# Optimization experiments

Hardware: AMD Instinct MI355X
Metric: run time of the kernel (lower is better)

The kernel has to match this reference:

```python
import jax, jax.numpy as jnp
import numpy as np

TOP_K = 2


def setup_inputs() -> dict:
    key = jax.random.key(0)
    ks = jax.random.split(key, 5)
    B, S, D, F, E = 2, 1024, 2048, 4096, 8
    scale_in = 1.0 / np.sqrt(D)
    scale_f = 1.0 / np.sqrt(F)
    return {
        "hidden_states": jax.random.normal(ks[0], (B, S, D), dtype=jnp.float32),
        "gate_w": jax.random.normal(ks[1], (D, E), dtype=jnp.float32) * scale_in,
        "w1": jax.random.normal(ks[2], (E, D, F), dtype=jnp.float32) * scale_in,
        "w3": jax.random.normal(ks[3], (E, D, F), dtype=jnp.float32) * scale_in,
        "w2": jax.random.normal(ks[4], (E, F, D), dtype=jnp.float32) * scale_f,
    }


def reference(hidden_states, gate_w, w1, w3, w2):
    orig_shape = hidden_states.shape
    D = orig_shape[-1]
    x = hidden_states.reshape(-1, D)                      # [T, D]
    E = gate_w.shape[-1]

    # Router: replicated linear (no bias), logits in fp32.
    router_logits = (x @ gate_w).astype(jnp.float32)      # [T, E]
    probs = jax.nn.softmax(router_logits, axis=-1)        # [T, E]
    topk_vals, topk_idx = jax.lax.top_k(probs, TOP_K)     # [T, K]
    # renormalize=False: use raw softmax probs of the selected experts.
    # Scatter top-k weights back to a dense [T, E] combine matrix.
    onehot = jax.nn.one_hot(topk_idx, E, dtype=probs.dtype)        # [T, K, E]
    combine = jnp.einsum("tke,tk->te", onehot, topk_vals)          # [T, E]

    # Dense-over-experts SwiGLU (reference for the fused grouped-GEMM).
    gate = jax.nn.silu(jnp.einsum("td,edf->etf", x, w1))  # [E, T, F]
    up = jnp.einsum("td,edf->etf", x, w3)                 # [E, T, F]
    expert_out = jnp.einsum("etf,efd->etd", gate * up, w2)  # [E, T, D]

    # Combine (this is the TP all-reduce + weighted sum in vllm).
    y = jnp.einsum("te,etd->td", combine, expert_out)     # [T, D]
    return y.reshape(orig_shape)
```

## Files before the change

### kernel.cpp

```cpp
#include <hip/hip_runtime.h>

typedef short v8s __attribute__((ext_vector_type(8)));
typedef float v4f __attribute__((ext_vector_type(4)));
typedef float v16f __attribute__((ext_vector_type(16)));

#define T_TOK 2048
#define DD 2048
#define FF 4096
#define EE 8
#define BM 128
#define BN 128
#define BK 64
#define MT_MAX 40
#define MAXROWS 5120

#define WS_COUNTS 0
#define WS_FILL   32
#define WS_ROWOFF 64
#define WS_TOPE   128
#define WS_TOPW   (WS_TOPE + T_TOK * 2 * 4)
#define WS_IDS    (WS_TOPW + T_TOK * 2 * 4)
#define WS_WTS    (WS_IDS + MAXROWS * 4)
#define WS_ZERO   (WS_WTS + MAXROWS * 4)
#define WS_XB     73984ul
#define WS_H      (WS_XB + 8388608ul)

#define SW(r)     ((((r) ^ ((r) >> 3)) & 7))
#define SWZ(r, kb) ((r) * 128 + ((kb) ^ (SW(r) << 4)))

#define VMCNTN(N) asm volatile("s_waitcnt vmcnt(" #N ")" ::: "memory")
#define VMCNT0()  asm volatile("s_waitcnt vmcnt(0)" ::: "memory")
#define LGKM0()   asm volatile("s_waitcnt lgkmcnt(0)" ::: "memory")
#define BARR()    __builtin_amdgcn_s_barrier()
#define SCHEDB()  __builtin_amdgcn_sched_barrier(0)

static __device__ __forceinline__ short f2bf(float f) {
  return __builtin_bit_cast(short, static_cast<__bf16>(f));
}

static __device__ __forceinline__ void gload_lds16(const void* g, void* l) {
  __builtin_amdgcn_global_load_lds(
      (const __attribute__((address_space(1))) unsigned int*)g,
      (__attribute__((address_space(3))) unsigned int*)l, 16, 0, 0);
}

__global__ __launch_bounds__(256) void xbf_k(const float* __restrict__ x,
                                             unsigned short* __restrict__ xb) {
  const int i = (blockIdx.x * 256 + threadIdx.x) * 8;
  v4f a = *(const v4f*)(x + i);
  v4f b = *(const v4f*)(x + i + 4);
  v8s h;
  h[0] = f2bf(a[0]); h[1] = f2bf(a[1]); h[2] = f2bf(a[2]); h[3] = f2bf(a[3]);
  h[4] = f2bf(b[0]); h[5] = f2bf(b[1]); h[6] = f2bf(b[2]); h[7] = f2bf(b[3]);
  *(v8s*)(xb + i) = h;
}

__global__ __launch_bounds__(256) void router_k(
    const float* __restrict__ x, const float* __restrict__ gw,
    int* __restrict__ counts, int* __restrict__ tope, float* __restrict__ topw) {
  const int lane = threadIdx.x & 63;
  const int t = blockIdx.x * 4 + (threadIdx.x >> 6);
  if (t >= T_TOK) return;
  float acc[EE] = {0.f, 0.f, 0.f, 0.f, 0.f, 0.f, 0.f, 0.f};
  const float* xr = x + (size_t)t * DD;
  for (int i = 0; i < DD / 64; ++i) {
    int k = i * 64 + lane;
    float xv = xr[k];
    const v4f* g = (const v4f*)(gw + (size_t)k * EE);
    v4f g0 = g[0], g1 = g[1];
    acc[0] += xv * g0[0]; acc[1] += xv * g0[1]; acc[2] += xv * g0[2]; acc[3] += xv * g0[3];
    acc[4] += xv * g1[0]; acc[5] += xv * g1[1]; acc[6] += xv * g1[2]; acc[7] += xv * g1[3];
  }
  #pragma unroll
  for (int e = 0; e < EE; ++e) {
    #pragma unroll
    for (int off = 32; off > 0; off >>= 1) acc[e] += __shfl_xor(acc[e], off);
  }
  if (lane == 0) {
    float m = acc[0];
    #pragma unroll
    for (int e = 1; e < EE; ++e) m = fmaxf(m, acc[e]);
    float p[EE], s = 0.f;
    #pragma unroll
    for (int e = 0; e < EE; ++e) { p[e] = expf(acc[e] - m); s += p[e]; }
    float inv = 1.f / s;
    #pragma unroll
    for (int e = 0; e < EE; ++e) p[e] *= inv;
    int e1 = 0;
    #pragma unroll
    for (int e = 1; e < EE; ++e) if (p[e] > p[e1]) e1 = e;
    int e2 = (e1 == 0) ? 1 : 0;
    #pragma unroll
    for (int e = 0; e < EE; ++e) if (e != e1 && p[e] > p[e2]) e2 = e;
    tope[2 * t] = e1;  tope[2 * t + 1] = e2;
    topw[2 * t] = p[e1]; topw[2 * t + 1] = p[e2];
    atomicAdd(&counts[e1], 1);
    atomicAdd(&counts[e2], 1);
  }
}

__global__ void offsets_k(const int* __restrict__ counts, int* __restrict__ rowoff) {
  if (threadIdx.x == 0) {
    int off = 0;
    #pragma unroll
    for (int e = 0; e < EE; ++e) {
      rowoff[e] = off;
      off += ((counts[e] + BM - 1) / BM) * BM;
    }
  }
}

__global__ __launch_bounds__(256) void scatter_k(
    const int* __restrict__ tope, const float* __restrict__ topw,
    const int* __restrict__ rowoff, int* __restrict__ fill,
    int* __restrict__ ids, float* __restrict__ wts) {
  const int t = blockIdx.x * 256 + threadIdx.x;
  if (t >= T_TOK) return;
  #pragma unroll
  for (int j = 0; j < 2; ++j) {
    int e = tope[2 * t + j];
    int pos = rowoff[e] + atomicAdd(&fill[e], 1);
    ids[pos] = t;
    wts[pos] = topw[2 * t + j];
  }
}

static __device__ __forceinline__ int find_expert(
    const int* counts, const int* rowoff, int mt) {
  int expert = -1;
  #pragma unroll
  for (int e = 0; e < EE; ++e) {
    int rs = rowoff[e];
    int tl = (counts[e] + BM - 1) / BM;
    if (mt * BM >= rs && mt * BM < rs + tl * BM) expert = e;
  }
  return expert;
}

static __device__ __forceinline__ void xcd_map(int* nt, int* mt) {
  int gx = gridDim.x, gy = gridDim.y;
  int nwg = gx * gy;
  int lin = blockIdx.y * gx + blockIdx.x;
  int q = nwg >> 3;
  int s = (lin & 7) * q + (lin >> 3);
  *nt = s / gy;
  *mt = s % gy;
}

__global__ __launch_bounds__(256, 2) void gemm1_k(
    const unsigned short* __restrict__ xb, const float* __restrict__ w1,
    const float* __restrict__ w3, const int* __restrict__ counts,
    const int* __restrict__ rowoff, const int* __restrict__ ids,
    unsigned short* __restrict__ H) {
  int nt, mt;
  xcd_map(&nt, &mt);
  const int expert = find_expert(counts, rowoff, mt);
  if (expert < 0) return;
  const int m0 = mt * BM, n0 = nt * BN;

  __shared__ unsigned short sA[BM * BK];
  __shared__ unsigned short sB0[BN * BK];
  __shared__ unsigned short sB1[BN * BK];

  const int tid = threadIdx.x;
  const int lane = tid & 63;
  const int wid = tid >> 6;
  const int wm = (wid >> 1) * 64, wn = (wid & 1) * 64;
  const int l32 = lane & 31;
  const int khi = lane >> 5;

  const unsigned short* ga[4];
  #pragma unroll
  for (int i = 0; i < 4; ++i) {
    int r = wid * 32 + i * 8 + (lane >> 3);
    ga[i] = xb + (size_t)ids[m0 + r] * DD + (((lane & 7) ^ SW(r)) << 3);
  }

  const int b_f4 = (tid & 31) * 4;
  const int b_k8 = (tid >> 5) * 8;
  const float* wb1 = w1 + (size_t)expert * DD * FF + n0 + b_f4 + (size_t)b_k8 * FF;
  const float* wb3 = w3 + (size_t)expert * DD * FF + n0 + b_f4 + (size_t)b_k8 * FF;

  v4f r1[8], r3[8];
  #define G1_ALDS(KT) { _Pragma("unroll") for (int i_ = 0; i_ < 4; ++i_)        \
      gload_lds16(ga[i_] + (size_t)(KT) * BK,                                   \
                  (char*)sA + (wid * 32 + i_ * 8) * 128); }
  #define G1_BL(KT) {                                                           \
      const float* p_ = wb1 + (size_t)(KT) * BK * FF;                           \
      _Pragma("unroll") for (int j_ = 0; j_ < 8; ++j_)                          \
        r1[j_] = *(const v4f*)(p_ + (size_t)j_ * FF);                           \
      p_ = wb3 + (size_t)(KT) * BK * FF;                                        \
      _Pragma("unroll") for (int j_ = 0; j_ < 8; ++j_)                          \
        r3[j_] = *(const v4f*)(p_ + (size_t)j_ * FF); }
  #define G1_BW() { _Pragma("unroll") for (int c_ = 0; c_ < 4; ++c_) {          \
      v8s h1_, h3_;                                                             \
      _Pragma("unroll") for (int j_ = 0; j_ < 8; ++j_) {                        \
        h1_[j_] = f2bf(r1[j_][c_]); h3_[j_] = f2bf(r3[j_][c_]); }               \
      *(v8s*)((char*)sB0 + SWZ(b_f4 + c_, b_k8 * 2)) = h1_;                     \
      *(v8s*)((char*)sB1 + SWZ(b_f4 + c_, b_k8 * 2)) = h3_; } }

  v16f acc1[2][2], acc3[2][2];
  #pragma unroll
  for (int i = 0; i < 2; ++i)
    #pragma unroll
    for (int j = 0; j < 2; ++j) {
      acc1[i][j] = (v16f)(0.f);
      acc3[i][j] = (v16f)(0.f);
    }

  G1_BL(0);

  for (int kt = 0; kt < DD / BK; ++kt) {
    G1_ALDS(kt);
    SCHEDB();
    G1_BW();
    if (kt + 1 < DD / BK) {
      G1_BL(kt + 1);
      SCHEDB();
      VMCNTN(16);
    } else {
      VMCNT0();
    }
    LGKM0(); BARR();
    SCHEDB();
    #pragma unroll
    for (int ks = 0; ks < 4; ++ks) {
      const int kb = (ks * 2 + khi) * 16;
      v8s a[2], b1[2], b3[2];
      #pragma unroll
      for (int m = 0; m < 2; ++m)
        a[m] = *(const v8s*)((const char*)sA + SWZ(wm + m * 32 + l32, kb));
      #pragma unroll
      for (int n = 0; n < 2; ++n) {
        b1[n] = *(const v8s*)((const char*)sB0 + SWZ(wn + n * 32 + l32, kb));
        b3[n] = *(const v8s*)((const char*)sB1 + SWZ(wn + n * 32 + l32, kb));
      }
      #pragma unroll
      for (int m = 0; m < 2; ++m)
        #pragma unroll
        for (int n = 0; n < 2; ++n) {
          acc1[m][n] = __builtin_amdgcn_mfma_f32_32x32x16_bf16(a[m], b1[n], acc1[m][n], 0, 0, 0);
          acc3[m][n] = __builtin_amdgcn_mfma_f32_32x32x16_bf16(a[m], b3[n], acc3[m][n], 0, 0, 0);
        }
    }
    BARR();
  }
  #pragma unroll
  for (int m = 0; m < 2; ++m)
    #pragma unroll
    for (int n = 0; n < 2; ++n)
      #pragma unroll
      for (int r = 0; r < 16; ++r) {
        int row = wm + m * 32 + (r & 3) + 8 * (r >> 2) + 4 * khi;
        int col = wn + n * 32 + l32;
        float g = acc1[m][n][r];
        float u = acc3[m][n][r];
        float hv = (g / (1.f + expf(-g))) * u;
        H[(size_t)(m0 + row) * FF + (n0 + col)] = (unsigned short)f2bf(hv);
      }
}

__global__ __launch_bounds__(256, 2) void gemm2_k(
    const unsigned short* __restrict__ H, const float* __restrict__ w2,
    const int* __restrict__ counts, const int* __restrict__ rowoff,
    const int* __restrict__ ids, const float* __restrict__ wts,
    float* __restrict__ out) {
  int nt, mt;
  xcd_map(&nt, &mt);
  const int expert = find_expert(counts, rowoff, mt);
  if (expert < 0) return;
  const int m0 = mt * BM, n0 = nt * BN;

  __shared__ unsigned short sA[BM * BK];
  __shared__ unsigned short sB[BN * BK];

  const int tid = threadIdx.x;
  const int lane = tid & 63;
  const int wid = tid >> 6;
  const int wm = (wid >> 1) * 64, wn = (wid & 1) * 64;
  const int l32 = lane & 31;
  const int khi = lane >> 5;

  const unsigned short* ga[4];
  #pragma unroll
  for (int i = 0; i < 4; ++i) {
    int r = wid * 32 + i * 8 + (lane >> 3);
    ga[i] = H + (size_t)(m0 + r) * FF + (((lane & 7) ^ SW(r)) << 3);
  }

  const int b_f4 = (tid & 31) * 4;
  const int b_k8 = (tid >> 5) * 8;
  const float* wb = w2 + (size_t)expert * FF * DD + n0 + b_f4 + (size_t)b_k8 * DD;

  v4f rb[8];
  #define G2_ALDS(KT) { _Pragma("unroll") for (int i_ = 0; i_ < 4; ++i_)        \
      gload_lds16(ga[i_] + (size_t)(KT) * BK,                                   \
                  (char*)sA + (wid * 32 + i_ * 8) * 128); }
  #define G2_BL(KT) { const float* p_ = wb + (size_t)(KT) * BK * DD;            \
      _Pragma("unroll") for (int j_ = 0; j_ < 8; ++j_)                          \
        rb[j_] = *(const v4f*)(p_ + (size_t)j_ * DD); }
  #define G2_BW() { _Pragma("unroll") for (int c_ = 0; c_ < 4; ++c_) {          \
      v8s h_;                                                                   \
      _Pragma("unroll") for (int j_ = 0; j_ < 8; ++j_) h_[j_] = f2bf(rb[j_][c_]);\
      *(v8s*)((char*)sB + SWZ(b_f4 + c_, b_k8 * 2)) = h_; } }

  v16f acc[2][2];
  #pragma unroll
  for (int i = 0; i < 2; ++i)
    #pragma unroll
    for (int j = 0; j < 2; ++j) acc[i][j] = (v16f)(0.f);

  G2_BL(0);

  for (int kt = 0; kt < FF / BK; ++kt) {
    G2_ALDS(kt);
    SCHEDB();
    G2_BW();
    if (kt + 1 < FF / BK) {
      G2_BL(kt + 1);
      SCHEDB();
      VMCNTN(8);
    } else {
      VMCNT0();
    }
    LGKM0(); BARR();
    SCHEDB();
    #pragma unroll
    for (int ks = 0; ks < 4; ++ks) {
      const int kb = (ks * 2 + khi) * 16;
      v8s a[2], b[2];
      #pragma unroll
      for (int m = 0; m < 2; ++m)
        a[m] = *(const v8s*)((const char*)sA + SWZ(wm + m * 32 + l32, kb));
      #pragma unroll
      for (int n = 0; n < 2; ++n)
        b[n] = *(const v8s*)((const char*)sB + SWZ(wn + n * 32 + l32, kb));
      #pragma unroll
      for (int m = 0; m < 2; ++m)
        #pragma unroll
        for (int n = 0; n < 2; ++n)
          acc[m][n] = __builtin_amdgcn_mfma_f32_32x32x16_bf16(a[m], b[n], acc[m][n], 0, 0, 0);
    }
    BARR();
  }
  #pragma unroll
  for (int m = 0; m < 2; ++m)
    #pragma unroll
    for (int r = 0; r < 16; ++r) {
      int row = m0 + wm + m * 32 + (r & 3) + 8 * (r >> 2) + 4 * khi;
      float wgt = wts[row];
      if (wgt != 0.f) {
        float* orow = out + (size_t)ids[row] * DD + n0 + wn + l32;
        #pragma unroll
        for (int n = 0; n < 2; ++n)
          atomicAdd(orow + n * 32, wgt * acc[m][n][r]);
      }
    }
}

extern "C" void kernel_launch(void* const* d_in, const int* in_sizes, int n_in,
                              void* d_out, int out_size, void* d_ws, size_t ws_size,
                              hipStream_t stream) {
  const float* x  = (const float*)d_in[0];
  const float* gw = (const float*)d_in[1];
  const float* w1 = (const float*)d_in[2];
  const float* w3 = (const float*)d_in[3];
  const float* w2 = (const float*)d_in[4];
  float* out = (float*)d_out;
  char* ws = (char*)d_ws;

  int*   counts = (int*)(ws + WS_COUNTS);
  int*   fill   = (int*)(ws + WS_FILL);
  int*   rowoff = (int*)(ws + WS_ROWOFF);
  int*   tope   = (int*)(ws + WS_TOPE);
  float* topw   = (float*)(ws + WS_TOPW);
  int*   ids    = (int*)(ws + WS_IDS);
  float* wts    = (float*)(ws + WS_WTS);
  unsigned short* xb = (unsigned short*)(ws + WS_XB);
  unsigned short* H  = (unsigned short*)(ws + WS_H);

  hipMemsetAsync(ws, 0, WS_ZERO, stream);
  hipMemsetAsync(d_out, 0, (size_t)out_size * sizeof(float), stream);

  xbf_k<<<T_TOK * DD / (256 * 8), 256, 0, stream>>>(x, xb);
  router_k<<<T_TOK / 4, 256, 0, stream>>>(x, gw, counts, tope, topw);
  offsets_k<<<1, 64, 0, stream>>>(counts, rowoff);
  scatter_k<<<T_TOK / 256, 256, 0, stream>>>(tope, topw, rowoff, fill, ids, wts);
  gemm1_k<<<dim3(FF / BN, MT_MAX), 256, 0, stream>>>(xb, w1, w3, counts, rowoff, ids, H);
  gemm2_k<<<dim3(DD / BN, MT_MAX), 256, 0, stream>>>(H, w2, counts, rowoff, ids, wts, out);
}
```

Baseline: 514.2 us.

## Replace gemm2 atomic scatter with bf16 staging buffer and combine kernel

gemm2 now writes each expert-row's output as bf16 into a dense staging buffer O instead of doing weighted float atomicAdds into the output. A new combine kernel reads each token's two slots (recorded by scatter) and computes the weighted sum, which also removes the output memset. This trades atomic contention for an extra kernel launch plus roughly 20 MB of extra write and read traffic, and rounds expert outputs to bf16 before combining.

```diff
diff --git a/kernel.cpp b/kernel.cpp
--- a/kernel.cpp
+++ b/kernel.cpp
@@ -22,13 +22,16 @@
 #define WS_IDS    (WS_TOPW + T_TOK * 2 * 4)
 #define WS_WTS    (WS_IDS + MAXROWS * 4)
 #define WS_ZERO   (WS_WTS + MAXROWS * 4)
-#define WS_XB     73984ul
+#define WS_SLOT   73856ul
+#define WS_XB     90368ul
 #define WS_H      (WS_XB + 8388608ul)
-
-#define SW(r)     ((((r) ^ ((r) >> 3)) & 7))
+#define WS_O      (WS_H + 41943040ul)
+
+#define SW(r)      ((((r) ^ ((r) >> 3)) & 7))
 #define SWZ(r, kb) ((r) * 128 + ((kb) ^ (SW(r) << 4)))
 
-#define VMCNTN(N) asm volatile("s_waitcnt vmcnt(" #N ")" ::: "memory")
+#define VMCNT16() asm volatile("s_waitcnt vmcnt(16)" ::: "memory")
+#define VMCNT8()  asm volatile("s_waitcnt vmcnt(8)" ::: "memory")
 #define VMCNT0()  asm volatile("s_waitcnt vmcnt(0)" ::: "memory")
 #define LGKM0()   asm volatile("s_waitcnt lgkmcnt(0)" ::: "memory")
 #define BARR()    __builtin_amdgcn_s_barrier()
@@ -36,6 +39,9 @@
 
 static __device__ __forceinline__ short f2bf(float f) {
   return __builtin_bit_cast(short, static_cast<__bf16>(f));
+}
+static __device__ __forceinline__ float bf2f(unsigned short u) {
+  return __builtin_bit_cast(float, ((unsigned)u) << 16);
 }
 
 static __device__ __forceinline__ void gload_lds16(const void* g, void* l) {
@@ -113,7 +119,7 @@
 __global__ __launch_bounds__(256) void scatter_k(
     const int* __restrict__ tope, const float* __restrict__ topw,
     const int* __restrict__ rowoff, int* __restrict__ fill,
-    int* __restrict__ ids, float* __restrict__ wts) {
+    int* __restrict__ ids, float* __restrict__ wts, int* __restrict__ slot) {
   const int t = blockIdx.x * 256 + threadIdx.x;
   if (t >= T_TOK) return;
   #pragma unroll
@@ -122,6 +128,7 @@
     int pos = rowoff[e] + atomicAdd(&fill[e], 1);
     ids[pos] = t;
     wts[pos] = topw[2 * t + j];
+    slot[2 * t + j] = pos;
   }
 }
 
@@ -217,7 +224,7 @@
     if (kt + 1 < DD / BK) {
       G1_BL(kt + 1);
       SCHEDB();
-      VMCNTN(16);
+      VMCNT16();
     } else {
       VMCNT0();
     }
@@ -263,8 +270,7 @@
 __global__ __launch_bounds__(256, 2) void gemm2_k(
     const unsigned short* __restrict__ H, const float* __restrict__ w2,
     const int* __restrict__ counts, const int* __restrict__ rowoff,
-    const int* __restrict__ ids, const float* __restrict__ wts,
-    float* __restrict__ out) {
+    unsigned short* __restrict__ O) {
   int nt, mt;
   xcd_map(&nt, &mt);
   const int expert = find_expert(counts, rowoff, mt);
@@ -319,7 +325,7 @@
     if (kt + 1 < FF / BK) {
       G2_BL(kt + 1);
       SCHEDB();
-      VMCNTN(8);
+      VMCNT8();
     } else {
       VMCNT0();
     }
@@ -343,19 +349,37 @@
     }
     BARR();
   }
+
   #pragma unroll
   for (int m = 0; m < 2; ++m)
     #pragma unroll
     for (int r = 0; r < 16; ++r) {
       int row = m0 + wm + m * 32 + (r & 3) + 8 * (r >> 2) + 4 * khi;
-      float wgt = wts[row];
-      if (wgt != 0.f) {
-        float* orow = out + (size_t)ids[row] * DD + n0 + wn + l32;
-        #pragma unroll
-        for (int n = 0; n < 2; ++n)
-          atomicAdd(orow + n * 32, wgt * acc[m][n][r]);
-      }
-    }
+      #pragma unroll
+      for (int n = 0; n < 2; ++n)
+        O[(size_t)row * DD + n0 + wn + n * 32 + l32] =
+            (unsigned short)f2bf(acc[m][n][r]);
+    }
+}
+
+__global__ __launch_bounds__(256) void combine_k(
+    const unsigned short* __restrict__ O, const int* __restrict__ slot,
+    const float* __restrict__ wts, float* __restrict__ out) {
+  const int t = blockIdx.x;
+  const int d = threadIdx.x * 8;
+  const int s0 = slot[2 * t], s1 = slot[2 * t + 1];
+  const float w0 = wts[s0], w1 = wts[s1];
+  v8s a = *(const v8s*)(O + (size_t)s0 * DD + d);
+  v8s b = *(const v8s*)(O + (size_t)s1 * DD + d);
+  v4f o0, o1;
+  #pragma unroll
+  for (int j = 0; j < 4; ++j) {
+    o0[j] = w0 * bf2f((unsigned short)a[j]) + w1 * bf2f((unsigned short)b[j]);
+    o1[j] = w0 * bf2f((unsigned short)a[j + 4]) + w1 * bf2f((unsigned short)b[j + 4]);
+  }
+  float* op = out + (size_t)t * DD + d;
+  *(v4f*)op = o0;
+  *(v4f*)(op + 4) = o1;
 }
 
 extern "C" void kernel_launch(void* const* d_in, const int* in_sizes, int n_in,
@@ -376,16 +400,18 @@
   float* topw   = (float*)(ws + WS_TOPW);
   int*   ids    = (int*)(ws + WS_IDS);
   float* wts    = (float*)(ws + WS_WTS);
+  int*   slot   = (int*)(ws + WS_SLOT);
   unsigned short* xb = (unsigned short*)(ws + WS_XB);
   unsigned short* H  = (unsigned short*)(ws + WS_H);
+  unsigned short* O  = (unsigned short*)(ws + WS_O);
 
   hipMemsetAsync(ws, 0, WS_ZERO, stream);
-  hipMemsetAsync(d_out, 0, (size_t)out_size * sizeof(float), stream);
 
   xbf_k<<<T_TOK * DD / (256 * 8), 256, 0, stream>>>(x, xb);
   router_k<<<T_TOK / 4, 256, 0, stream>>>(x, gw, counts, tope, topw);
   offsets_k<<<1, 64, 0, stream>>>(counts, rowoff);
-  scatter_k<<<T_TOK / 256, 256, 0, stream>>>(tope, topw, rowoff, fill, ids, wts);
+  scatter_k<<<T_TOK / 256, 256, 0, stream>>>(tope, topw, rowoff, fill, ids, wts, slot);
   gemm1_k<<<dim3(FF / BN, MT_MAX), 256, 0, stream>>>(xb, w1, w3, counts, rowoff, ids, H);
-  gemm2_k<<<dim3(DD / BN, MT_MAX), 256, 0, stream>>>(H, w2, counts, rowoff, ids, wts, out);
-}
+  gemm2_k<<<dim3(DD / BN, MT_MAX), 256, 0, stream>>>(H, w2, counts, rowoff, O);
+  combine_k<<<T_TOK, 256, 0, stream>>>(O, slot, wts, out);
+}
```

Measured after the change: 496.9 us (median of 2 runs). 1.03x faster.
